# Kernel tuning notes

Hardware: AMD Instinct MI355X
Metric: run time of the kernel (lower is better)

Reference implementation:

```python
import jax, jax.numpy as jnp
import numpy as np

# World configuration (2D layout ['h','w'])
B = 16            # batch
NH, NW = 64, 64   # token grid (token_sizes)
DO = 768          # dim_in + dim_coords
KH, KW = 16, 16   # kernel_sizes (patch extent, overlapping)
SH, SW = 8, 8     # patch_sizes (strides)
H, WF = 512, 512  # field_sizes
E = H * WF        # world.num_elements


def _build_fold_index():
    # idx[h, w, dh, dw] = clamp(h*SH+dh, 0, H-1)*WF + clamp(w*SW+dw, 0, WF-1)
    # mirrors FieldDecoder._build_fold_index with grid strides (WF, 1)
    ph = np.clip(np.arange(NH)[:, None] * SH + np.arange(KH)[None, :], 0, H - 1)   # [NH,KH]
    pw = np.clip(np.arange(NW)[:, None] * SW + np.arange(KW)[None, :], 0, WF - 1)  # [NW,KW]
    idx = ph[:, None, :, None] * WF + pw[None, :, None, :]                          # [NH,NW,KH,KW]
    return jnp.asarray(idx.reshape(-1), dtype=jnp.int32)


def setup_inputs() -> dict:
    key = jax.random.key(0)
    k1, k2 = jax.random.split(key)
    tgt = jax.random.normal(k1, (B, NH * NW, DO), dtype=jnp.float32)
    weight = jax.random.normal(k2, (KH, KW, DO), dtype=jnp.float32) * 0.02  # EinMix weight (k=v=1 absorbed)
    idx = _build_fold_index()
    return {"tgt": tgt, "weight": weight, "idx": idx}


def reference(tgt, weight, idx):
    # EinMix: 'b (h w) do -> b (h w hh ww)'  (shared per-patch projection, k=v=1)
    proj = jnp.einsum('bnd,xyd->bnxy', tgt, weight)          # [B, NH*NW, KH, KW]
    proj = proj.reshape(B, -1)                                # flat order (h, w, hh, ww) == idx layout
    # scatter_reduce(reduce='mean', include_self=False): sum then divide by counts
    sums = jnp.zeros((B, E), proj.dtype).at[:, idx].add(proj)
    counts = jnp.zeros((E,), proj.dtype).at[idx].add(1.0)     # every element is covered (kernel >= stride)
    field = sums / jnp.maximum(counts, 1.0)
    # unflatten_fields: 'b (flat) -> b h w'
    return field.reshape(B, H, WF)
```

## Files before the change

kernel.cpp:

```cpp
#include <hip/hip_runtime.h>
#include <hip/hip_bf16.h>

#define DIM      768
#define NPATCH   4096
#define BATCH    16
#define MROWS    65536
#define NCOLS    256

typedef __attribute__((ext_vector_type(8))) short bf16x8;
typedef __attribute__((ext_vector_type(4))) float f32x4;

static __device__ __forceinline__ unsigned short f2bf(float f) {
    union { float f; unsigned int u; } v; v.f = f;
    unsigned int u = v.u;
    return (unsigned short)((u + 0x7FFFu + ((u >> 16) & 1u)) >> 16);
}
static __device__ __forceinline__ float bf2f(unsigned int u16) {
    union { unsigned int i; float f; } x; x.i = u16 << 16; return x.f;
}
static __device__ __forceinline__ bf16x8 pack_bf8(float4 a, float4 b) {
    union { bf16x8 v; unsigned int u[4]; } r;
    r.u[0] = (unsigned)f2bf(a.x) | ((unsigned)f2bf(a.y) << 16);
    r.u[1] = (unsigned)f2bf(a.z) | ((unsigned)f2bf(a.w) << 16);
    r.u[2] = (unsigned)f2bf(b.x) | ((unsigned)f2bf(b.y) << 16);
    r.u[3] = (unsigned)f2bf(b.z) | ((unsigned)f2bf(b.w) << 16);
    return r.v;
}

__global__ void wpack_kernel(const float* __restrict__ w, unsigned short* __restrict__ wf) {
    const int t    = blockIdx.x * blockDim.x + threadIdx.x;
    const int lane = t & 63;
    const int j    = (t >> 6) & 15;
    const int kk   = t >> 10;
    const int n    = j * 16 + (lane & 15);
    const int k    = kk * 32 + (lane >> 4) * 8;
    const float* src = w + (size_t)n * DIM + k;
    float4 v0 = *(const float4*)src;
    float4 v1 = *(const float4*)(src + 4);
    union { bf16x8 v; uint4 q; } o;
    o.v = pack_bf8(v0, v1);
    *(uint4*)(wf + (size_t)t * 8) = o.q;
}

__global__ __launch_bounds__(256, 2) void gemm_kernel(const float* __restrict__ A,
                                                      const unsigned short* __restrict__ Bf,
                                                      unsigned short* __restrict__ Cb) {
    __shared__ unsigned short sC[4 * 32 * 256];

    const int tid  = threadIdx.x;
    const int w    = tid >> 6;
    const int lane = tid & 63;
    const int l15  = lane & 15;
    const int quad = lane >> 4;
    const int m0   = blockIdx.x * 128;

    f32x4 acc[2][16] = {};

    const float* a0 = A + (size_t)(m0 + w * 32 + l15) * DIM + quad * 8;
    const float* a1 = a0 + (size_t)16 * DIM;
    const uint4* bp = (const uint4*)Bf + lane;

    #pragma unroll 2
    for (int kk = 0; kk < 24; ++kk) {
        const float4 r00 = *(const float4*)(a0 + kk * 32);
        const float4 r01 = *(const float4*)(a0 + kk * 32 + 4);
        const float4 r10 = *(const float4*)(a1 + kk * 32);
        const float4 r11 = *(const float4*)(a1 + kk * 32 + 4);
        const bf16x8 af0 = pack_bf8(r00, r01);
        const bf16x8 af1 = pack_bf8(r10, r11);
        #pragma unroll
        for (int j = 0; j < 16; ++j) {
            union { uint4 q; bf16x8 v; } b;
            b.q = bp[(kk * 16 + j) * 64];
            acc[0][j] = __builtin_amdgcn_mfma_f32_16x16x32_bf16(af0, b.v, acc[0][j], 0, 0, 0);
            acc[1][j] = __builtin_amdgcn_mfma_f32_16x16x32_bf16(af1, b.v, acc[1][j], 0, 0, 0);
        }
    }

    unsigned short* reg = sC + w * (32 * 256);
    #pragma unroll
    for (int i = 0; i < 2; ++i)
        #pragma unroll
        for (int j = 0; j < 16; ++j)
            #pragma unroll
            for (int rr = 0; rr < 4; ++rr)
                reg[(i * 16 + quad * 4 + rr) * 256 + j * 16 + l15] = f2bf(acc[i][j][rr]);
    __syncthreads();

    const int orow = tid >> 3;
    const int ou   = tid & 7;
    #pragma unroll
    for (int rb = 0; rb < 4; ++rb) {
        const int row = orow + rb * 32;
        const unsigned short* src = sC + row * 256 + ou * 32;
        unsigned short* dst = Cb + (size_t)(m0 + row) * NCOLS + ou * 32;
        #pragma unroll
        for (int q = 0; q < 4; ++q)
            *(uint4*)(dst + q * 8) = *(const uint4*)(src + q * 8);
    }
}

__global__ __launch_bounds__(256) void gather_kernel(const unsigned short* __restrict__ proj,
                                                     float* __restrict__ out) {
    __shared__ unsigned short sCur[64 * 256];
    __shared__ unsigned short sPrevHi[64 * 128];

    const int blk = blockIdx.x;
    const int b   = blk >> 6;
    const int h   = blk & 63;
    const int tid = threadIdx.x;
    const unsigned short* base = proj + (size_t)b * (NPATCH * NCOLS);

    const uint4* gCur = (const uint4*)(base + (size_t)h * 64 * 256);
    #pragma unroll
    for (int p = 0; p < 8; ++p)
        ((uint4*)sCur)[tid + p * 256] = gCur[tid + p * 256];
    if (h > 0) {
        const uint4* gPrev = (const uint4*)(base + (size_t)(h - 1) * 64 * 256);
        #pragma unroll
        for (int p = 0; p < 4; ++p) {
            int i = tid + p * 256;
            ((uint4*)sPrevHi)[i] = gPrev[(i >> 4) * 32 + 16 + (i & 15)];
        }
    }
    __syncthreads();

    const int r  = tid >> 5;
    const int cg = tid & 31;
    const int ph = h * 8 + r;
    const float inv_ch = (h == 0) ? 1.f : ((ph == 511) ? 0.1f : 0.5f);

    float res[16];
    #pragma unroll
    for (int j = 0; j < 16; ++j) {
        const int pw = cg * 16 + j;
        const int w1 = pw >> 3, dw = pw & 7;
        float v = bf2f(sCur[w1 * 256 + r * 16 + dw]);
        if (pw >= 8) v += bf2f(sCur[(w1 - 1) * 256 + r * 16 + dw + 8]);
        if (h > 0) {
            v += bf2f(sPrevHi[w1 * 128 + r * 16 + dw]);
            if (pw >= 8) v += bf2f(sPrevHi[(w1 - 1) * 128 + r * 16 + dw + 8]);
        }
        if (pw == 511) {
            #pragma unroll
            for (int dwe = 8; dwe < 16; ++dwe) {
                v += bf2f(sCur[63 * 256 + r * 16 + dwe]);
                if (h > 0) v += bf2f(sPrevHi[63 * 128 + r * 16 + dwe]);
            }
        }
        if (ph == 511) {
            #pragma unroll 1
            for (int dh = 8; dh < 16; ++dh) {
                float e = bf2f(sCur[w1 * 256 + dh * 16 + dw]);
                if (pw >= 8) e += bf2f(sCur[(w1 - 1) * 256 + dh * 16 + dw + 8]);
                if (pw == 511) {
                    #pragma unroll
                    for (int dwe = 8; dwe < 16; ++dwe)
                        e += bf2f(sCur[63 * 256 + dh * 16 + dwe]);
                }
                v += e;
            }
        }
        const float inv_cw = (pw < 8) ? 1.f : ((pw == 511) ? 0.1f : 0.5f);
        res[j] = v * inv_ch * inv_cw;
    }

    float* orow = out + ((size_t)(b * 512 + ph)) * 512 + cg * 16;
    #pragma unroll
    for (int q = 0; q < 4; ++q)
        *(float4*)(orow + q * 4) = make_float4(res[4 * q], res[4 * q + 1], res[4 * q + 2], res[4 * q + 3]);
}

extern "C" void kernel_launch(void* const* d_in, const int* in_sizes, int n_in,
                              void* d_out, int out_size, void* d_ws, size_t ws_size,
                              hipStream_t stream) {
    const float* tgt    = (const float*)d_in[0];
    const float* weight = (const float*)d_in[1];
    float* out = (float*)d_out;

    unsigned short* proj = (unsigned short*)d_ws;
    unsigned short* wf   = (unsigned short*)((char*)d_ws + (size_t)MROWS * NCOLS * 2);

    wpack_kernel<<<96, 256, 0, stream>>>(weight, wf);
    gemm_kernel<<<MROWS / 128, 256, 0, stream>>>(tgt, wf, proj);
    gather_kernel<<<BATCH * 64, 256, 0, stream>>>(proj, out);
}
```

Baseline: 372.1 us.

## Stage weight tiles in LDS for GEMM and vectorize padded gather reads

After: 323.0 us. 13.2% less time.

```diff
diff --git a/kernel.cpp b/kernel.cpp
--- a/kernel.cpp
+++ b/kernel.cpp
@@ -45,7 +45,7 @@
 __global__ __launch_bounds__(256, 2) void gemm_kernel(const float* __restrict__ A,
                                                       const unsigned short* __restrict__ Bf,
                                                       unsigned short* __restrict__ Cb) {
-    __shared__ unsigned short sC[4 * 32 * 256];
+    __shared__ unsigned short smem[128 * 256];
 
     const int tid  = threadIdx.x;
     const int w    = tid >> 6;
@@ -58,33 +58,44 @@
 
     const float* a0 = A + (size_t)(m0 + w * 32 + l15) * DIM + quad * 8;
     const float* a1 = a0 + (size_t)16 * DIM;
-    const uint4* bp = (const uint4*)Bf + lane;
-
-    #pragma unroll 2
-    for (int kk = 0; kk < 24; ++kk) {
-        const float4 r00 = *(const float4*)(a0 + kk * 32);
-        const float4 r01 = *(const float4*)(a0 + kk * 32 + 4);
-        const float4 r10 = *(const float4*)(a1 + kk * 32);
-        const float4 r11 = *(const float4*)(a1 + kk * 32 + 4);
-        const bf16x8 af0 = pack_bf8(r00, r01);
-        const bf16x8 af1 = pack_bf8(r10, r11);
-        #pragma unroll
-        for (int j = 0; j < 16; ++j) {
-            union { uint4 q; bf16x8 v; } b;
-            b.q = bp[(kk * 16 + j) * 64];
-            acc[0][j] = __builtin_amdgcn_mfma_f32_16x16x32_bf16(af0, b.v, acc[0][j], 0, 0, 0);
-            acc[1][j] = __builtin_amdgcn_mfma_f32_16x16x32_bf16(af1, b.v, acc[1][j], 0, 0, 0);
-        }
-    }
-
-    unsigned short* reg = sC + w * (32 * 256);
+
+    for (int c = 0; c < 6; ++c) {
+        __syncthreads();
+        {
+            const uint4* src = (const uint4*)Bf + c * 4096 + tid;
+            uint4* dst = (uint4*)smem + tid;
+            #pragma unroll 4
+            for (int s = 0; s < 16; ++s)
+                dst[s * 256] = src[s * 256];
+        }
+        __syncthreads();
+
+        #pragma unroll
+        for (int kk = 0; kk < 4; ++kk) {
+            const int kg = c * 4 + kk;
+            const float4 r00 = *(const float4*)(a0 + kg * 32);
+            const float4 r01 = *(const float4*)(a0 + kg * 32 + 4);
+            const float4 r10 = *(const float4*)(a1 + kg * 32);
+            const float4 r11 = *(const float4*)(a1 + kg * 32 + 4);
+            const bf16x8 af0 = pack_bf8(r00, r01);
+            const bf16x8 af1 = pack_bf8(r10, r11);
+            #pragma unroll
+            for (int j = 0; j < 16; ++j) {
+                const bf16x8 b = *(const bf16x8*)(smem + ((kk * 16 + j) * 64 + lane) * 8);
+                acc[0][j] = __builtin_amdgcn_mfma_f32_16x16x32_bf16(af0, b, acc[0][j], 0, 0, 0);
+                acc[1][j] = __builtin_amdgcn_mfma_f32_16x16x32_bf16(af1, b, acc[1][j], 0, 0, 0);
+            }
+        }
+    }
+
+    __syncthreads();
     #pragma unroll
     for (int i = 0; i < 2; ++i)
         #pragma unroll
         for (int j = 0; j < 16; ++j)
             #pragma unroll
             for (int rr = 0; rr < 4; ++rr)
-                reg[(i * 16 + quad * 4 + rr) * 256 + j * 16 + l15] = f2bf(acc[i][j][rr]);
+                smem[(w * 32 + i * 16 + quad * 4 + rr) * 256 + j * 16 + l15] = f2bf(acc[i][j][rr]);
     __syncthreads();
 
     const int orow = tid >> 3;
@@ -92,7 +103,7 @@
     #pragma unroll
     for (int rb = 0; rb < 4; ++rb) {
         const int row = orow + rb * 32;
-        const unsigned short* src = sC + row * 256 + ou * 32;
+        const unsigned short* src = smem + row * 256 + ou * 32;
         unsigned short* dst = Cb + (size_t)(m0 + row) * NCOLS + ou * 32;
         #pragma unroll
         for (int q = 0; q < 4; ++q)
@@ -100,10 +111,12 @@
     }
 }
 
-__global__ __launch_bounds__(256) void gather_kernel(const unsigned short* __restrict__ proj,
-                                                     float* __restrict__ out) {
-    __shared__ unsigned short sCur[64 * 256];
-    __shared__ unsigned short sPrevHi[64 * 128];
+#define CSTRG 280
+#define PSTRG 152
+__global__ __launch_bounds__(256, 2) void gather_kernel(const unsigned short* __restrict__ proj,
+                                                        float* __restrict__ out) {
+    __shared__ unsigned short sCur[64 * CSTRG];
+    __shared__ unsigned short sPrevHi[64 * PSTRG];
 
     const int blk = blockIdx.x;
     const int b   = blk >> 6;
@@ -113,62 +126,76 @@
 
     const uint4* gCur = (const uint4*)(base + (size_t)h * 64 * 256);
     #pragma unroll
-    for (int p = 0; p < 8; ++p)
-        ((uint4*)sCur)[tid + p * 256] = gCur[tid + p * 256];
+    for (int p = 0; p < 8; ++p) {
+        const int i = tid + p * 256;
+        *(uint4*)(sCur + (i >> 5) * CSTRG + (i & 31) * 8) = gCur[i];
+    }
     if (h > 0) {
         const uint4* gPrev = (const uint4*)(base + (size_t)(h - 1) * 64 * 256);
         #pragma unroll
         for (int p = 0; p < 4; ++p) {
-            int i = tid + p * 256;
-            ((uint4*)sPrevHi)[i] = gPrev[(i >> 4) * 32 + 16 + (i & 15)];
+            const int i = tid + p * 256;
+            *(uint4*)(sPrevHi + (i >> 4) * PSTRG + (i & 15) * 8) = gPrev[(i >> 4) * 32 + 16 + (i & 15)];
         }
     }
     __syncthreads();
 
-    const int r  = tid >> 5;
-    const int cg = tid & 31;
-    const int ph = h * 8 + r;
-    const float inv_ch = (h == 0) ? 1.f : ((ph == 511) ? 0.1f : 0.5f);
-
-    float res[16];
-    #pragma unroll
-    for (int j = 0; j < 16; ++j) {
-        const int pw = cg * 16 + j;
-        const int w1 = pw >> 3, dw = pw & 7;
-        float v = bf2f(sCur[w1 * 256 + r * 16 + dw]);
-        if (pw >= 8) v += bf2f(sCur[(w1 - 1) * 256 + r * 16 + dw + 8]);
+    const float fch_base = (h == 0) ? 1.f : 0.5f;
+
+    #pragma unroll
+    for (int t = 0; t < 2; ++t) {
+        const int task = tid + t * 256;
+        const int r  = task >> 6;
+        const int wg = task & 63;
+        const int ph = h * 8 + r;
+
+        float s[8] = {0.f, 0.f, 0.f, 0.f, 0.f, 0.f, 0.f, 0.f};
+        auto addq = [&](uint4 v) {
+            const unsigned int u[4] = {v.x, v.y, v.z, v.w};
+            #pragma unroll
+            for (int q = 0; q < 4; ++q) {
+                s[2 * q]     += bf2f(u[q] & 0xFFFFu);
+                s[2 * q + 1] += bf2f(u[q] >> 16);
+            }
+        };
+        auto sumq = [&](uint4 v) -> float {
+            const unsigned int u[4] = {v.x, v.y, v.z, v.w};
+            float e = 0.f;
+            #pragma unroll
+            for (int q = 0; q < 4; ++q) e += bf2f(u[q] & 0xFFFFu) + bf2f(u[q] >> 16);
+            return e;
+        };
+
+        addq(*(const uint4*)(sCur + wg * CSTRG + r * 16));
+        if (wg > 0) addq(*(const uint4*)(sCur + (wg - 1) * CSTRG + r * 16 + 8));
         if (h > 0) {
-            v += bf2f(sPrevHi[w1 * 128 + r * 16 + dw]);
-            if (pw >= 8) v += bf2f(sPrevHi[(w1 - 1) * 128 + r * 16 + dw + 8]);
-        }
-        if (pw == 511) {
-            #pragma unroll
-            for (int dwe = 8; dwe < 16; ++dwe) {
-                v += bf2f(sCur[63 * 256 + r * 16 + dwe]);
-                if (h > 0) v += bf2f(sPrevHi[63 * 128 + r * 16 + dwe]);
-            }
-        }
+            addq(*(const uint4*)(sPrevHi + wg * PSTRG + r * 16));
+            if (wg > 0) addq(*(const uint4*)(sPrevHi + (wg - 1) * PSTRG + r * 16 + 8));
+        }
+        if (wg == 63) {
+            s[7] += sumq(*(const uint4*)(sCur + 63 * CSTRG + r * 16 + 8));
+            if (h > 0) s[7] += sumq(*(const uint4*)(sPrevHi + 63 * PSTRG + r * 16 + 8));
+        }
+        float fch = fch_base;
         if (ph == 511) {
+            fch = 0.1f;
             #pragma unroll 1
             for (int dh = 8; dh < 16; ++dh) {
-                float e = bf2f(sCur[w1 * 256 + dh * 16 + dw]);
-                if (pw >= 8) e += bf2f(sCur[(w1 - 1) * 256 + dh * 16 + dw + 8]);
-                if (pw == 511) {
-                    #pragma unroll
-                    for (int dwe = 8; dwe < 16; ++dwe)
-                        e += bf2f(sCur[63 * 256 + dh * 16 + dwe]);
-                }
-                v += e;
+                addq(*(const uint4*)(sCur + wg * CSTRG + dh * 16));
+                if (wg > 0) addq(*(const uint4*)(sCur + (wg - 1) * CSTRG + dh * 16 + 8));
+                if (wg == 63) s[7] += sumq(*(const uint4*)(sCur + 63 * CSTRG + dh * 16 + 8));
             }
         }
-        const float inv_cw = (pw < 8) ? 1.f : ((pw == 511) ? 0.1f : 0.5f);
-        res[j] = v * inv_ch * inv_cw;
-    }
-
-    float* orow = out + ((size_t)(b * 512 + ph)) * 512 + cg * 16;
-    #pragma unroll
-    for (int q = 0; q < 4; ++q)
-        *(float4*)(orow + q * 4) = make_float4(res[4 * q], res[4 * q + 1], res[4 * q + 2], res[4 * q + 3]);
+
+        const float fcw = (wg == 0) ? 1.f : 0.5f;
+        float f7 = fcw;
+        if (wg == 63) f7 = 0.1f;
+        float* orow = out + ((size_t)(b * 512 + ph)) * 512 + wg * 8;
+        *(float4*)orow       = make_float4(s[0] * fch * fcw, s[1] * fch * fcw,
+                                           s[2] * fch * fcw, s[3] * fch * fcw);
+        *(float4*)(orow + 4) = make_float4(s[4] * fch * fcw, s[5] * fch * fcw,
+                                           s[6] * fch * fcw, s[7] * fch * f7);
+    }
 }
 
 extern "C" void kernel_launch(void* const* d_in, const int* in_sizes, int n_in,
```
